# Kernel optimization log

Measured on AMD Instinct MI355X. Metric: run time of the kernel, lower is better.

Reference implementation:

```python
import jax, jax.numpy as jnp
import numpy as np

V, D, H, L, S, B, FF, MAXLEN = 50257, 768, 12, 12, 1024, 4, 3072, 1024
HD = D // H
EPS = 1e-5


def layernorm(x, w, b):
    m = jnp.mean(x, axis=-1, keepdims=True)
    v = jnp.mean(jnp.square(x - m), axis=-1, keepdims=True)
    return (x - m) * jax.lax.rsqrt(v + EPS) * w + b


def setup_inputs() -> dict:
    key = jax.random.key(0)
    ks = jax.random.split(key, 8)
    std = 0.02
    return {
        "tokens": jax.random.randint(ks[0], (B, S), 0, V, dtype=jnp.int32),
        "wte": std * jax.random.normal(ks[1], (V, D), jnp.float32),
        "wpe": std * jax.random.normal(ks[2], (1, MAXLEN, D), jnp.float32),
        "ln1_w": jnp.ones((L, D), jnp.float32),
        "ln1_b": jnp.zeros((L, D), jnp.float32),
        "ln2_w": jnp.ones((L, D), jnp.float32),
        "ln2_b": jnp.zeros((L, D), jnp.float32),
        "W_exp": std * jax.random.normal(ks[3], (L, D, 3 * D), jnp.float32),
        "b_exp": jnp.zeros((L, 3 * D), jnp.float32),
        "W_o": std * jax.random.normal(ks[4], (L, D, D), jnp.float32),
        "b_o": jnp.zeros((L, D), jnp.float32),
        "W_ff1": std * jax.random.normal(ks[5], (L, D, FF), jnp.float32),
        "b_ff1": jnp.zeros((L, FF), jnp.float32),
        "W_ff2": std * jax.random.normal(ks[6], (L, FF, D), jnp.float32),
        "b_ff2": jnp.zeros((L, D), jnp.float32),
    }


def reference(tokens, wte, wpe, ln1_w, ln1_b, ln2_w, ln2_b,
              W_exp, b_exp, W_o, b_o, W_ff1, b_ff1, W_ff2, b_ff2):
    Bc, Sc = tokens.shape
    x = wte[tokens] + wpe[:, :Sc, :]                      # [B,S,D]
    mask = jnp.tril(jnp.ones((Sc, Sc), bool))             # causal (past=None)
    scale = 1.0 / jnp.sqrt(jnp.float32(HD))
    presents = []
    for l in range(L):
        h = layernorm(x, ln1_w[l], ln1_b[l])
        qkv = h @ W_exp[l] + b_exp[l]                     # [B,S,3D]
        q, k, v = jnp.split(qkv, 3, axis=-1)
        q = q.reshape(Bc, Sc, H, HD)
        k = k.reshape(Bc, Sc, H, HD)
        v = v.reshape(Bc, Sc, H, HD)
        presents.append(jnp.stack([k, v]))                # [2,B,S,H,HD]
        score = jnp.einsum('bqhd,bkhd->bhqk', q, k)
        score = jnp.where(mask, score, jnp.float32(-1e20))
        attn = jax.nn.softmax(score * scale, axis=-1)     # mask applied BEFORE scaling, as in source
        a = jnp.einsum('bhqk,bkhd->bqhd', attn, v).reshape(Bc, Sc, D)
        a = a @ W_o[l] + b_o[l]
        add = layernorm(a + x, ln2_w[l], ln2_b[l])        # LN2 on residual sum (GPT2-variant in source)
        ff = jax.nn.gelu(add @ W_ff1[l] + b_ff1[l], approximate=False)
        ff = ff @ W_ff2[l] + b_ff2[l]
        x = ff + add
    return x, jnp.stack(presents)                         # [L,2,B,S,H,HD]
```

## Files before the change

kernel.cpp:

```cpp
#include <hip/hip_runtime.h>
#include <hip/hip_bf16.h>
#include <math.h>

#define Bc 4
#define Sc 1024
#define Dc 768
#define Hc 12
#define Lc 12
#define FFc 3072
#define Mtot (Bc*Sc)

typedef __bf16 bf16x8 __attribute__((ext_vector_type(8)));
typedef float f32x4 __attribute__((ext_vector_type(4)));

__device__ __forceinline__ void gload_lds16(const void* g, void* l) {
    __builtin_amdgcn_global_load_lds((const __attribute__((address_space(1))) void*)g,
                                     (__attribute__((address_space(3))) void*)l, 16, 0, 0);
}

template <int N>
__device__ __forceinline__ void waitcnt_vm() {
    if constexpr (N == 0)      asm volatile("s_waitcnt vmcnt(0)" ::: "memory");
    else if constexpr (N == 4) asm volatile("s_waitcnt vmcnt(4)" ::: "memory");
    else if constexpr (N == 5) asm volatile("s_waitcnt vmcnt(5)" ::: "memory");
    else if constexpr (N == 6) asm volatile("s_waitcnt vmcnt(6)" ::: "memory");
    else static_assert(N == 0, "unsupported vmcnt");
}

__global__ __launch_bounds__(256) void embed_kernel(const int* __restrict__ tokens,
                                                    const float* __restrict__ wte,
                                                    const float* __restrict__ wpe,
                                                    float* __restrict__ x) {
    int row = blockIdx.x;
    int s = row & (Sc - 1);
    int tok = tokens[row];
    const float* wt = wte + (size_t)tok * Dc;
    const float* wp = wpe + (size_t)s * Dc;
    float* xr = x + (size_t)row * Dc;
#pragma unroll
    for (int k = 0; k < 3; ++k) {
        int d = threadIdx.x + k * 256;
        xr[d] = wt[d] + wp[d];
    }
}

__global__ __launch_bounds__(256) void transpose_all_kernel(
        const float* __restrict__ We, const float* __restrict__ Wo,
        const float* __restrict__ Wf1, const float* __restrict__ Wf2,
        __bf16* __restrict__ Te, __bf16* __restrict__ To,
        __bf16* __restrict__ Tf1, __bf16* __restrict__ Tf2) {
    __shared__ float tl[32][33];
    int bid = blockIdx.x;
    const float* W; __bf16* T; int K, N, t;
    if (bid < 1728)      { W = We;  T = Te;  K = 768;  N = 2304; t = bid; }
    else if (bid < 2304) { W = Wo;  T = To;  K = 768;  N = 768;  t = bid - 1728; }
    else if (bid < 4608) { W = Wf1; T = Tf1; K = 768;  N = 3072; t = bid - 2304; }
    else                 { W = Wf2; T = Tf2; K = 3072; N = 768;  t = bid - 4608; }
    int nx = N >> 5;
    int n0 = (t % nx) * 32, k0 = (t / nx) * 32;
    int tx = threadIdx.x & 31, ty = threadIdx.x >> 5;
#pragma unroll
    for (int i = 0; i < 4; ++i)
        tl[ty + 8 * i][tx] = W[(size_t)(k0 + ty + 8 * i) * N + n0 + tx];
    __syncthreads();
#pragma unroll
    for (int i = 0; i < 4; ++i)
        T[(size_t)(n0 + ty + 8 * i) * K + k0 + tx] = (__bf16)tl[tx][ty + 8 * i];
}

template <bool DUAL>
__global__ __launch_bounds__(256) void ln_kernel(const float* __restrict__ x,
                                                 const float* __restrict__ lw,
                                                 const float* __restrict__ lb,
                                                 __bf16* __restrict__ outb,
                                                 float* __restrict__ outf) {
    int row = blockIdx.x;
    const float* xr = x + (size_t)row * Dc;
    int t = threadIdx.x;
    float v0 = xr[t], v1 = xr[t + 256], v2 = xr[t + 512];
    float s1 = v0 + v1 + v2;
    float s2 = v0 * v0 + v1 * v1 + v2 * v2;
    __shared__ float red[8];
#pragma unroll
    for (int o = 32; o; o >>= 1) {
        s1 += __shfl_down(s1, o);
        s2 += __shfl_down(s2, o);
    }
    int wv = t >> 6;
    if ((t & 63) == 0) { red[wv] = s1; red[4 + wv] = s2; }
    __syncthreads();
    float S1 = red[0] + red[1] + red[2] + red[3];
    float S2 = red[4] + red[5] + red[6] + red[7];
    float mean = S1 * (1.0f / Dc);
    float var = S2 * (1.0f / Dc) - mean * mean;
    float rs = rsqrtf(var + 1e-5f);
    size_t ro = (size_t)row * Dc;
    float o0 = (v0 - mean) * rs * lw[t]       + lb[t];
    float o1 = (v1 - mean) * rs * lw[t + 256] + lb[t + 256];
    float o2 = (v2 - mean) * rs * lw[t + 512] + lb[t + 512];
    outb[ro + t]       = (__bf16)o0;
    outb[ro + t + 256] = (__bf16)o1;
    outb[ro + t + 512] = (__bf16)o2;
    if (DUAL) {
        outf[ro + t]       = o0;
        outf[ro + t + 256] = o1;
        outf[ro + t + 512] = o2;
    }
}

template <int BMr, int BNc, int BK, int EPI>
__global__ __launch_bounds__(256) void gemm_bf16(const __bf16* __restrict__ A,
                                                 const __bf16* __restrict__ BT,
                                                 const float* __restrict__ bias,
                                                 const float* __restrict__ addin,
                                                 float* __restrict__ Cf,
                                                 __bf16* __restrict__ Cb,
                                                 float* __restrict__ pres,
                                                 int K, int N) {
    constexpr int HRm = BMr / 32, HRn = BNc / 32;
    constexpr int KS  = BK / 32;
    constexpr int LPR = BK / 8;
    constexpr int SSH = (BK == 32) ? 1 : 0;
    constexpr int IA  = BMr * BK / 2048;
    constexpr int IB  = BNc * BK / 2048;
    static_assert(IA * 2048 == BMr * BK && IB * 2048 == BNc * BK, "staging granularity");
    __shared__ __bf16 As[2][BMr * BK];
    __shared__ __bf16 Bs[2][BNc * BK];
    int tid = threadIdx.x;
    int w = tid >> 6, l = tid & 63;
    int wrow = (w >> 1) * (BMr / 2), wcol = (w & 1) * (BNc / 2);
    int brow0 = blockIdx.x * BMr, bcol0 = blockIdx.y * BNc;
    int rsel = l & 15, lg = l >> 4;

    f32x4 acc[HRm][HRn] = {};

    const __bf16* Abase = A + (size_t)brow0 * K;
    const __bf16* Bbase = BT + (size_t)bcol0 * K;

    auto stage = [&](int buf, int kt) {
#pragma unroll
        for (int i = 0; i < IA; ++i) {
            int cid = i * 256 + tid;
            int row = cid / LPR, slot = cid % LPR;
            int chunk = slot ^ ((row >> SSH) & (LPR - 1));
            gload_lds16(Abase + (size_t)row * K + kt + chunk * 8,
                        &As[buf][(i * 256 + w * 64) * 8]);
        }
#pragma unroll
        for (int i = 0; i < IB; ++i) {
            int cid = i * 256 + tid;
            int row = cid / LPR, slot = cid % LPR;
            int chunk = slot ^ ((row >> SSH) & (LPR - 1));
            gload_lds16(Bbase + (size_t)row * K + kt + chunk * 8,
                        &Bs[buf][(i * 256 + w * 64) * 8]);
        }
    };

    stage(0, 0);
    int nk = K / BK;
    for (int kt = 0; kt < nk; ++kt) {
        int cur = kt & 1;
        if (kt + 1 < nk) {
            stage(cur ^ 1, (kt + 1) * BK);
            waitcnt_vm<IA + IB>();
        } else {
            waitcnt_vm<0>();
        }
        __builtin_amdgcn_s_barrier();
        __builtin_amdgcn_sched_barrier(0);

        bf16x8 af[KS][HRm], bfr[KS][HRn];
#pragma unroll
        for (int m = 0; m < HRm; ++m) {
            int r = wrow + m * 16 + rsel;
            int sw = (r >> SSH) & (LPR - 1);
#pragma unroll
            for (int s = 0; s < KS; ++s)
                af[s][m] = *(const bf16x8*)(&As[cur][r * BK + ((s * 4 + lg) ^ sw) * 8]);
        }
#pragma unroll
        for (int n = 0; n < HRn; ++n) {
            int r = wcol + n * 16 + rsel;
            int sw = (r >> SSH) & (LPR - 1);
#pragma unroll
            for (int s = 0; s < KS; ++s)
                bfr[s][n] = *(const bf16x8*)(&Bs[cur][r * BK + ((s * 4 + lg) ^ sw) * 8]);
        }
#pragma unroll
        for (int s = 0; s < KS; ++s)
#pragma unroll
            for (int m = 0; m < HRm; ++m)
#pragma unroll
                for (int n = 0; n < HRn; ++n)
                    acc[m][n] = __builtin_amdgcn_mfma_f32_16x16x32_bf16(af[s][m], bfr[s][n], acc[m][n], 0, 0, 0);

        __builtin_amdgcn_sched_barrier(0);
        __builtin_amdgcn_s_barrier();
    }

    int r4 = lg * 4, cc = rsel;
#pragma unroll
    for (int m = 0; m < HRm; ++m)
#pragma unroll
        for (int n = 0; n < HRn; ++n) {
            int col = bcol0 + wcol + n * 16 + cc;
            float bv = bias[col];
#pragma unroll
            for (int i = 0; i < 4; ++i) {
                int row = brow0 + wrow + m * 16 + r4 + i;
                float v = acc[m][n][i] + bv;
                if (EPI == 1) {
                    v += addin[(size_t)row * N + col];
                    Cf[(size_t)row * N + col] = v;
                }
                if (EPI == 2) {
                    float u = 0.7978845608f * (v + 0.044715f * v * v * v);
                    v = v / (1.0f + __expf(-2.0f * u));
                    Cb[(size_t)row * N + col] = (__bf16)v;
                }
                if (EPI == 3) {
                    Cb[(size_t)row * N + col] = (__bf16)v;
                    if (col >= 768) {
                        int kv = (col >= 1536) ? 1 : 0;
                        pres[((size_t)kv * Mtot + row) * Dc + (col - 768 - kv * 768)] = v;
                    }
                }
            }
        }
}

__global__ __launch_bounds__(256) void attn_mfma_kernel(const __bf16* __restrict__ qkvb,
                                                        __bf16* __restrict__ aout) {
    __shared__ __bf16 Ks[64 * 72];
    __shared__ __bf16 Vts[64 * 72];
    __shared__ __bf16 Ps[4][16 * 72];
    int bh = blockIdx.x;
    int b = bh / Hc, h = bh % Hc;
    int qt = (Sc / 64 - 1) - blockIdx.y;
    int tid = threadIdx.x;
    int w = tid >> 6, l = tid & 63;
    int lr = l & 15, lg = l >> 4;
    int qb = qt * 64;

    const __bf16* base = qkvb + (size_t)b * Sc * 2304 + h * 64;

    bf16x8 qf[2];
    {
        const __bf16* qrow = base + (size_t)(qb + w * 16 + lr) * 2304 + lg * 8;
        qf[0] = *(const bf16x8*)(qrow);
        qf[1] = *(const bf16x8*)(qrow + 32);
    }

    f32x4 O[4] = {};
    float mrow[4], lrowv[4];
#pragma unroll
    for (int i = 0; i < 4; ++i) { mrow[i] = -1e30f; lrowv[i] = 0.0f; }

    int kj = tid >> 2, kc = tid & 3;
    int vj = tid & 63, vd0 = (tid >> 6) * 8;

    for (int t = 0; t <= qt; ++t) {
        __syncthreads();
#pragma unroll
        for (int it = 0; it < 2; ++it) {
            int c = kc + 4 * it;
            bf16x8 v = *(const bf16x8*)(base + (size_t)(t * 64 + kj) * 2304 + 768 + c * 8);
            *(bf16x8*)(&Ks[kj * 72 + c * 8]) = v;
        }
#pragma unroll
        for (int it = 0; it < 2; ++it) {
            int d0 = vd0 + 32 * it;
            bf16x8 v = *(const bf16x8*)(base + (size_t)(t * 64 + vj) * 2304 + 1536 + d0);
#pragma unroll
            for (int i = 0; i < 8; ++i)
                Vts[(d0 + i) * 72 + vj] = v[i];
        }
        __syncthreads();

        f32x4 sc[4] = {};
        __builtin_amdgcn_s_setprio(1);
#pragma unroll
        for (int s = 0; s < 2; ++s)
#pragma unroll
            for (int n = 0; n < 4; ++n) {
                bf16x8 kf = *(const bf16x8*)(&Ks[(n * 16 + lr) * 72 + s * 32 + lg * 8]);
                sc[n] = __builtin_amdgcn_mfma_f32_16x16x32_bf16(qf[s], kf, sc[n], 0, 0, 0);
            }
        __builtin_amdgcn_s_setprio(0);

        bool diag = (t == qt);
#pragma unroll
        for (int n = 0; n < 4; ++n)
#pragma unroll
            for (int i = 0; i < 4; ++i) {
                float s = sc[n][i] * 0.125f;
                if (diag) {
                    int jg = n * 16 + lr;
                    int qg = w * 16 + lg * 4 + i;
                    if (jg > qg) s = -1e30f;
                }
                sc[n][i] = s;
            }
        float corr[4], psum[4];
#pragma unroll
        for (int i = 0; i < 4; ++i) {
            float mx = fmaxf(fmaxf(sc[0][i], sc[1][i]), fmaxf(sc[2][i], sc[3][i]));
#pragma unroll
            for (int o = 1; o < 16; o <<= 1) mx = fmaxf(mx, __shfl_xor(mx, o));
            float mnew = fmaxf(mrow[i], mx);
            corr[i] = __expf(mrow[i] - mnew);
            mrow[i] = mnew;
            psum[i] = 0.0f;
        }
#pragma unroll
        for (int n = 0; n < 4; ++n)
#pragma unroll
            for (int i = 0; i < 4; ++i) {
                float p = __expf(sc[n][i] - mrow[i]);
                psum[i] += p;
                Ps[w][(lg * 4 + i) * 72 + n * 16 + lr] = (__bf16)p;
            }
#pragma unroll
        for (int i = 0; i < 4; ++i) {
#pragma unroll
            for (int o = 1; o < 16; o <<= 1) psum[i] += __shfl_xor(psum[i], o);
            lrowv[i] = lrowv[i] * corr[i] + psum[i];
        }
#pragma unroll
        for (int n = 0; n < 4; ++n)
#pragma unroll
            for (int i = 0; i < 4; ++i) O[n][i] *= corr[i];
        __builtin_amdgcn_s_setprio(1);
#pragma unroll
        for (int s = 0; s < 2; ++s) {
            bf16x8 pf = *(const bf16x8*)(&Ps[w][lr * 72 + s * 32 + lg * 8]);
#pragma unroll
            for (int n = 0; n < 4; ++n) {
                bf16x8 vf = *(const bf16x8*)(&Vts[(n * 16 + lr) * 72 + s * 32 + lg * 8]);
                O[n] = __builtin_amdgcn_mfma_f32_16x16x32_bf16(pf, vf, O[n], 0, 0, 0);
            }
        }
        __builtin_amdgcn_s_setprio(0);
    }
    __bf16* orow = aout + (size_t)(b * Sc + qb + w * 16 + lg * 4) * Dc + h * 64 + lr;
#pragma unroll
    for (int n = 0; n < 4; ++n)
#pragma unroll
        for (int i = 0; i < 4; ++i)
            orow[(size_t)i * Dc + n * 16] = (__bf16)(O[n][i] / lrowv[i]);
}

extern "C" void kernel_launch(void* const* d_in, const int* in_sizes, int n_in,
                              void* d_out, int out_size, void* d_ws, size_t ws_size,
                              hipStream_t stream) {
    const int*   tokens = (const int*)d_in[0];
    const float* wte    = (const float*)d_in[1];
    const float* wpe    = (const float*)d_in[2];
    const float* ln1_w  = (const float*)d_in[3];
    const float* ln1_b  = (const float*)d_in[4];
    const float* ln2_w  = (const float*)d_in[5];
    const float* ln2_b  = (const float*)d_in[6];
    const float* W_exp  = (const float*)d_in[7];
    const float* b_exp  = (const float*)d_in[8];
    const float* W_o    = (const float*)d_in[9];
    const float* b_o    = (const float*)d_in[10];
    const float* W_ff1  = (const float*)d_in[11];
    const float* b_ff1  = (const float*)d_in[12];
    const float* W_ff2  = (const float*)d_in[13];
    const float* b_ff2  = (const float*)d_in[14];

    float* out_x    = (float*)d_out;
    float* out_pres = out_x + (size_t)Mtot * Dc;

    float* ws   = (float*)d_ws;
    float* x    = ws;
    float* addf = x + (size_t)Mtot * Dc;
    __bf16* hb   = (__bf16*)(addf + (size_t)Mtot * Dc);
    __bf16* addb = hb + (size_t)Mtot * Dc;
    __bf16* qkvb = addb + (size_t)Mtot * Dc;
    __bf16* ff1b = qkvb + (size_t)Mtot * 3 * Dc;
    __bf16* wt_exp = ff1b + (size_t)Mtot * FFc;
    __bf16* wt_o   = wt_exp + (size_t)2304 * 768;
    __bf16* wt_ff1 = wt_o   + (size_t)768 * 768;
    __bf16* wt_ff2 = wt_ff1 + (size_t)3072 * 768;

    embed_kernel<<<Mtot, 256, 0, stream>>>(tokens, wte, wpe, x);

    for (int lidx = 0; lidx < Lc; ++lidx) {
        transpose_all_kernel<<<6912, 256, 0, stream>>>(
            W_exp + (size_t)lidx * 768 * 2304, W_o + (size_t)lidx * 768 * 768,
            W_ff1 + (size_t)lidx * 768 * 3072, W_ff2 + (size_t)lidx * 3072 * 768,
            wt_exp, wt_o, wt_ff1, wt_ff2);

        ln_kernel<false><<<Mtot, 256, 0, stream>>>(
            x, ln1_w + lidx * Dc, ln1_b + lidx * Dc, hb, nullptr);
        gemm_bf16<64, 192, 32, 3><<<dim3(Mtot / 64, 2304 / 192), 256, 0, stream>>>(
            hb, wt_exp, b_exp + (size_t)lidx * 3 * Dc,
            nullptr, nullptr, qkvb, out_pres + (size_t)lidx * 2 * Mtot * Dc, 768, 2304);
        attn_mfma_kernel<<<dim3(Bc * Hc, Sc / 64), 256, 0, stream>>>(qkvb, hb);
        gemm_bf16<64, 96, 64, 1><<<dim3(Mtot / 64, 768 / 96), 256, 0, stream>>>(
            hb, wt_o, b_o + (size_t)lidx * Dc,
            x, x, nullptr, nullptr, 768, 768);
        ln_kernel<true><<<Mtot, 256, 0, stream>>>(
            x, ln2_w + lidx * Dc, ln2_b + lidx * Dc, addb, addf);
        gemm_bf16<128, 128, 32, 2><<<dim3(Mtot / 128, FFc / 128), 256, 0, stream>>>(
            addb, wt_ff1, b_ff1 + (size_t)lidx * FFc,
            nullptr, nullptr, ff1b, nullptr, 768, FFc);
        float* ff2dst = (lidx == Lc - 1) ? out_x : x;
        gemm_bf16<64, 96, 64, 1><<<dim3(Mtot / 64, 768 / 96), 256, 0, stream>>>(
            ff1b, wt_ff2, b_ff2 + (size_t)lidx * Dc,
            addf, ff2dst, nullptr, nullptr, 3072, 768);
    }
}
```

Baseline: 2.071 ms.

## Triple-buffer GEMM K-loop and fuse LN1 into weight transpose kernel

The GEMM main loop moves from double to triple buffering in LDS, keeping two stages of async global-to-LDS loads in flight. It waits with vmcnt of two stages' worth of loads instead of one. Separately, the per-layer weight transpose and the first layernorm are merged into one launch, with extra blocks doing the LN rows. This removes a kernel launch per layer and lets the two independent jobs overlap. The extra LDS buffer raises shared-memory use per block and may reduce occupancy for the larger tile configs.

```diff
diff --git a/kernel.cpp b/kernel.cpp
--- a/kernel.cpp
+++ b/kernel.cpp
@@ -20,10 +20,11 @@
 
 template <int N>
 __device__ __forceinline__ void waitcnt_vm() {
-    if constexpr (N == 0)      asm volatile("s_waitcnt vmcnt(0)" ::: "memory");
-    else if constexpr (N == 4) asm volatile("s_waitcnt vmcnt(4)" ::: "memory");
-    else if constexpr (N == 5) asm volatile("s_waitcnt vmcnt(5)" ::: "memory");
-    else if constexpr (N == 6) asm volatile("s_waitcnt vmcnt(6)" ::: "memory");
+    if constexpr (N == 0)       asm volatile("s_waitcnt vmcnt(0)" ::: "memory");
+    else if constexpr (N == 4)  asm volatile("s_waitcnt vmcnt(4)" ::: "memory");
+    else if constexpr (N == 5)  asm volatile("s_waitcnt vmcnt(5)" ::: "memory");
+    else if constexpr (N == 8)  asm volatile("s_waitcnt vmcnt(8)" ::: "memory");
+    else if constexpr (N == 10) asm volatile("s_waitcnt vmcnt(10)" ::: "memory");
     else static_assert(N == 0, "unsupported vmcnt");
 }
 
@@ -44,31 +45,58 @@
     }
 }
 
-__global__ __launch_bounds__(256) void transpose_all_kernel(
+__global__ __launch_bounds__(256) void prep_kernel(
         const float* __restrict__ We, const float* __restrict__ Wo,
         const float* __restrict__ Wf1, const float* __restrict__ Wf2,
         __bf16* __restrict__ Te, __bf16* __restrict__ To,
-        __bf16* __restrict__ Tf1, __bf16* __restrict__ Tf2) {
-    __shared__ float tl[32][33];
+        __bf16* __restrict__ Tf1, __bf16* __restrict__ Tf2,
+        const float* __restrict__ x, const float* __restrict__ lw,
+        const float* __restrict__ lb, __bf16* __restrict__ outb) {
+    __shared__ float shm[32 * 33];
     int bid = blockIdx.x;
-    const float* W; __bf16* T; int K, N, t;
-    if (bid < 1728)      { W = We;  T = Te;  K = 768;  N = 2304; t = bid; }
-    else if (bid < 2304) { W = Wo;  T = To;  K = 768;  N = 768;  t = bid - 1728; }
-    else if (bid < 4608) { W = Wf1; T = Tf1; K = 768;  N = 3072; t = bid - 2304; }
-    else                 { W = Wf2; T = Tf2; K = 3072; N = 768;  t = bid - 4608; }
-    int nx = N >> 5;
-    int n0 = (t % nx) * 32, k0 = (t / nx) * 32;
-    int tx = threadIdx.x & 31, ty = threadIdx.x >> 5;
-#pragma unroll
-    for (int i = 0; i < 4; ++i)
-        tl[ty + 8 * i][tx] = W[(size_t)(k0 + ty + 8 * i) * N + n0 + tx];
-    __syncthreads();
-#pragma unroll
-    for (int i = 0; i < 4; ++i)
-        T[(size_t)(n0 + ty + 8 * i) * K + k0 + tx] = (__bf16)tl[tx][ty + 8 * i];
-}
-
-template <bool DUAL>
+    if (bid < 6912) {
+        const float* W; __bf16* T; int K, N, t;
+        if (bid < 1728)      { W = We;  T = Te;  K = 768;  N = 2304; t = bid; }
+        else if (bid < 2304) { W = Wo;  T = To;  K = 768;  N = 768;  t = bid - 1728; }
+        else if (bid < 4608) { W = Wf1; T = Tf1; K = 768;  N = 3072; t = bid - 2304; }
+        else                 { W = Wf2; T = Tf2; K = 3072; N = 768;  t = bid - 4608; }
+        int nx = N >> 5;
+        int n0 = (t % nx) * 32, k0 = (t / nx) * 32;
+        int tx = threadIdx.x & 31, ty = threadIdx.x >> 5;
+#pragma unroll
+        for (int i = 0; i < 4; ++i)
+            shm[(ty + 8 * i) * 33 + tx] = W[(size_t)(k0 + ty + 8 * i) * N + n0 + tx];
+        __syncthreads();
+#pragma unroll
+        for (int i = 0; i < 4; ++i)
+            T[(size_t)(n0 + ty + 8 * i) * K + k0 + tx] = (__bf16)shm[tx * 33 + ty + 8 * i];
+    } else {
+        int row = bid - 6912;
+        const float* xr = x + (size_t)row * Dc;
+        int t = threadIdx.x;
+        float v0 = xr[t], v1 = xr[t + 256], v2 = xr[t + 512];
+        float s1 = v0 + v1 + v2;
+        float s2 = v0 * v0 + v1 * v1 + v2 * v2;
+#pragma unroll
+        for (int o = 32; o; o >>= 1) {
+            s1 += __shfl_down(s1, o);
+            s2 += __shfl_down(s2, o);
+        }
+        int wv = t >> 6;
+        if ((t & 63) == 0) { shm[wv] = s1; shm[4 + wv] = s2; }
+        __syncthreads();
+        float S1 = shm[0] + shm[1] + shm[2] + shm[3];
+        float S2 = shm[4] + shm[5] + shm[6] + shm[7];
+        float mean = S1 * (1.0f / Dc);
+        float var = S2 * (1.0f / Dc) - mean * mean;
+        float rs = rsqrtf(var + 1e-5f);
+        size_t ro = (size_t)row * Dc;
+        outb[ro + t]       = (__bf16)((v0 - mean) * rs * lw[t]       + lb[t]);
+        outb[ro + t + 256] = (__bf16)((v1 - mean) * rs * lw[t + 256] + lb[t + 256]);
+        outb[ro + t + 512] = (__bf16)((v2 - mean) * rs * lw[t + 512] + lb[t + 512]);
+    }
+}
+
 __global__ __launch_bounds__(256) void ln_kernel(const float* __restrict__ x,
                                                  const float* __restrict__ lw,
                                                  const float* __restrict__ lb,
@@ -101,11 +129,9 @@
     outb[ro + t]       = (__bf16)o0;
     outb[ro + t + 256] = (__bf16)o1;
     outb[ro + t + 512] = (__bf16)o2;
-    if (DUAL) {
-        outf[ro + t]       = o0;
-        outf[ro + t + 256] = o1;
-        outf[ro + t + 512] = o2;
-    }
+    outf[ro + t]       = o0;
+    outf[ro + t + 256] = o1;
+    outf[ro + t + 512] = o2;
 }
 
 template <int BMr, int BNc, int BK, int EPI>
@@ -123,9 +149,10 @@
     constexpr int SSH = (BK == 32) ? 1 : 0;
     constexpr int IA  = BMr * BK / 2048;
     constexpr int IB  = BNc * BK / 2048;
+    constexpr int S1w = IA + IB;
     static_assert(IA * 2048 == BMr * BK && IB * 2048 == BNc * BK, "staging granularity");
-    __shared__ __bf16 As[2][BMr * BK];
-    __shared__ __bf16 Bs[2][BNc * BK];
+    __shared__ __bf16 As[3][BMr * BK];
+    __shared__ __bf16 Bs[3][BNc * BK];
     int tid = threadIdx.x;
     int w = tid >> 6, l = tid & 63;
     int wrow = (w >> 1) * (BMr / 2), wcol = (w & 1) * (BNc / 2);
@@ -156,13 +183,17 @@
         }
     };
 
+    int nk = K / BK;
     stage(0, 0);
-    int nk = K / BK;
+    stage(1, BK);
+    int cur = 0;
     for (int kt = 0; kt < nk; ++kt) {
-        int cur = kt & 1;
-        if (kt + 1 < nk) {
-            stage(cur ^ 1, (kt + 1) * BK);
-            waitcnt_vm<IA + IB>();
+        if (kt + 2 < nk) {
+            int b2 = cur + 2; if (b2 >= 3) b2 -= 3;
+            stage(b2, (kt + 2) * BK);
+            waitcnt_vm<2 * S1w>();
+        } else if (kt + 1 < nk) {
+            waitcnt_vm<S1w>();
         } else {
             waitcnt_vm<0>();
         }
@@ -196,6 +227,7 @@
 
         __builtin_amdgcn_sched_barrier(0);
         __builtin_amdgcn_s_barrier();
+        cur = (cur == 2) ? 0 : cur + 1;
     }
 
     int r4 = lg * 4, cc = rsel;
@@ -387,13 +419,12 @@
     embed_kernel<<<Mtot, 256, 0, stream>>>(tokens, wte, wpe, x);
 
     for (int lidx = 0; lidx < Lc; ++lidx) {
-        transpose_all_kernel<<<6912, 256, 0, stream>>>(
+        prep_kernel<<<6912 + Mtot, 256, 0, stream>>>(
             W_exp + (size_t)lidx * 768 * 2304, W_o + (size_t)lidx * 768 * 768,
             W_ff1 + (size_t)lidx * 768 * 3072, W_ff2 + (size_t)lidx * 3072 * 768,
-            wt_exp, wt_o, wt_ff1, wt_ff2);
-
-        ln_kernel<false><<<Mtot, 256, 0, stream>>>(
-            x, ln1_w + lidx * Dc, ln1_b + lidx * Dc, hb, nullptr);
+            wt_exp, wt_o, wt_ff1, wt_ff2,
+            x, ln1_w + lidx * Dc, ln1_b + lidx * Dc, hb);
+
         gemm_bf16<64, 192, 32, 3><<<dim3(Mtot / 64, 2304 / 192), 256, 0, stream>>>(
             hb, wt_exp, b_exp + (size_t)lidx * 3 * Dc,
             nullptr, nullptr, qkvb, out_pres + (size_t)lidx * 2 * Mtot * Dc, 768, 2304);
@@ -401,7 +432,7 @@
         gemm_bf16<64, 96, 64, 1><<<dim3(Mtot / 64, 768 / 96), 256, 0, stream>>>(
             hb, wt_o, b_o + (size_t)lidx * Dc,
             x, x, nullptr, nullptr, 768, 768);
-        ln_kernel<true><<<Mtot, 256, 0, stream>>>(
+        ln_kernel<<<Mtot, 256, 0, stream>>>(
             x, ln2_w + lidx * Dc, ln2_b + lidx * Dc, addb, addf);
         gemm_bf16<128, 128, 32, 2><<<dim3(Mtot / 128, FFc / 128), 256, 0, stream>>>(
             addb, wt_ff1, b_ff1 + (size_t)lidx * FFc,
```

Measured after the change: 2.032 ms. About the same (-1.9%).
